# Kernel tuning notes

Hardware: AMD Instinct MI355X
Metric: run time of the kernel (lower is better)

## Reference

```python
import jax, jax.numpy as jnp
import numpy as np

NUM_LAYERS = 3


def setup_inputs() -> dict:
    key = jax.random.key(0)
    ks = jax.random.split(key, 12)
    N, E, D_IN, D, ED = 50000, 800000, 6, 64, 4
    return {
        "x": jax.random.normal(ks[0], (N, D_IN), dtype=jnp.float32),
        "edge_index": jax.random.randint(ks[1], (2, E), 0, N, dtype=jnp.int64),
        "edge_attr": jax.random.normal(ks[2], (E, ED), dtype=jnp.float32),
        "z_soft": jax.random.uniform(ks[3], (E, ED), dtype=jnp.float32),
        "W_nt": jax.random.normal(ks[4], (D, D_IN), dtype=jnp.float32) * 0.1,
        "b_nt": jax.random.normal(ks[5], (D,), dtype=jnp.float32) * 0.1,
        "weight": jax.random.normal(ks[6], (NUM_LAYERS, D, D), dtype=jnp.float32) * 0.1,
        "W_ih": jax.random.normal(ks[7], (3 * D, D), dtype=jnp.float32) * 0.1,
        "W_hh": jax.random.normal(ks[8], (3 * D, D), dtype=jnp.float32) * 0.1,
        "b_ih": jax.random.normal(ks[9], (3 * D,), dtype=jnp.float32) * 0.1,
        "b_hh": jax.random.normal(ks[10], (3 * D,), dtype=jnp.float32) * 0.1,
    }


def gru_cell(m, h, W_ih, W_hh, b_ih, b_hh):
    # PyTorch GRUCell: gates ordered (r, z, n)
    gi = m @ W_ih.T + b_ih
    gh = h @ W_hh.T + b_hh
    i_r, i_z, i_n = jnp.split(gi, 3, axis=-1)
    h_r, h_z, h_n = jnp.split(gh, 3, axis=-1)
    r = jax.nn.sigmoid(i_r + h_r)
    z = jax.nn.sigmoid(i_z + h_z)
    n = jnp.tanh(i_n + r * h_n)
    return (1.0 - z) * n + z * h


def reference(x, edge_index, edge_attr, z_soft, W_nt, b_nt, weight, W_ih, W_hh, b_ih, b_hh):
    # node_transform: Linear + ReLU
    h = jax.nn.relu(x @ W_nt.T + b_nt)  # [N, D]
    # edge_attr gating (faithful to source; unused since edge_weight=None)
    _ = z_soft * edge_attr
    src, dst = edge_index[0], edge_index[1]
    N = h.shape[0]
    for i in range(NUM_LAYERS):
        m = h @ weight[i]                                   # [N, D]
        agg = jax.ops.segment_sum(m[src], dst, num_segments=N)  # gather-scatter add
        h = gru_cell(agg, h, W_ih, W_hh, b_ih, b_hh)
    return h
```

## Files before the change

kernel.cpp:

```cpp
#include <hip/hip_runtime.h>
#include <hip/hip_bf16.h>
#include <stdint.h>

#define D 64
typedef __hip_bfloat16 bf16;
typedef unsigned short u16;
typedef __attribute__((ext_vector_type(8))) short bf16x8;
typedef __attribute__((ext_vector_type(4))) float f32x4;

__device__ __forceinline__ float bf2f(u16 u) { return __uint_as_float(((uint32_t)u) << 16); }
__device__ __forceinline__ u16 f2bf(float f) { return __bfloat16_as_ushort(__float2bfloat16(f)); }

template <bool F32>
__device__ __forceinline__ float ld(const void* p, int i) {
    if constexpr (F32) return ((const float*)p)[i];
    else return bf2f(((const u16*)p)[i]);
}

__global__ __launch_bounds__(256) void detect_kernel(const void* x, const int* ei, int* flags) {
    __shared__ float smax[256];
    __shared__ int sor[256];
    int t = threadIdx.x;
    const u16* xs = (const u16*)x;
    float mx = 0.f;
#pragma unroll
    for (int i = 0; i < 16; ++i) {
        float a = fabsf(bf2f(xs[t * 16 + i]));
        if (!(a == a)) a = 1e30f;
        mx = fmaxf(mx, a);
    }
    int any = 0;
#pragma unroll
    for (int i = 0; i < 8; ++i) any |= ei[2 * (t * 8 + i) + 1];
    smax[t] = mx; sor[t] = any;
    __syncthreads();
    for (int s = 128; s > 0; s >>= 1) {
        if (t < s) { smax[t] = fmaxf(smax[t], smax[t + s]); sor[t] |= sor[t + s]; }
        __syncthreads();
    }
    if (t == 0) { flags[0] = (smax[0] > 1000.f) ? 1 : 0; flags[1] = (sor[0] != 0) ? 1 : 0; }
}

__global__ __launch_bounds__(256) void convert_edges(const int* __restrict__ flags,
                                                     const int* __restrict__ ei,
                                                     uint32_t* __restrict__ pe, int E, int N) {
    int i0 = blockIdx.x * 1024 + threadIdx.x;
    bool i32 = flags[1] != 0;
#pragma unroll
    for (int u = 0; u < 4; ++u) {
        int i = i0 + u * 256;
        if (i < E) {
            int src, dst;
            if (i32) { src = ei[i];     dst = ei[E + i]; }
            else     { src = ei[2 * i]; dst = ei[2 * (E + i)]; }
            uint32_t v;
            if ((unsigned)src >= (unsigned)N || (unsigned)dst >= (unsigned)N) v = 0xFFFFFFFFu;
            else v = (uint32_t)(u16)src | ((uint32_t)dst << 16);
            pe[i] = v;
        }
    }
}

#define N_WCT 36864
#define N_WTH 12288
#define N_B   384
template <bool F32>
__device__ __forceinline__ void nt_body(const void* x, const void* Wnt, const void* bnt,
                                        u16* ht, int N, int blk) {
    int gid = blk * 256 + threadIdx.x;
    if (gid >= N * D) return;
    int n = gid >> 6, c = gid & 63;
    float acc = ld<F32>(bnt, c);
#pragma unroll
    for (int k = 0; k < 6; ++k)
        acc = fmaf(ld<F32>(x, n * 6 + k), ld<F32>(Wnt, c * 6 + k), acc);
    ht[gid] = f2bf(fmaxf(acc, 0.f));
}
template <bool F32>
__device__ __forceinline__ void wc_body(const void* W, const void* Wih, const void* Whh,
                                        const void* bih, const void* bhh,
                                        u16* WCh, u16* WCl, u16* WVh, u16* WVl,
                                        float* B, int blk) {
    int i = blk * 256 + threadIdx.x;
    if (i < N_WCT) {
        int l = i / 12288, rem = i % 12288, k = rem / 192, r = rem % 192;
        float acc = 0.f;
#pragma unroll 8
        for (int j = 0; j < 64; ++j)
            acc = fmaf(ld<F32>(W, l * 4096 + k * 64 + j), ld<F32>(Wih, r * 64 + j), acc);
        u16 hi = f2bf(acc);
        WCh[l * 12288 + r * 64 + k] = hi;
        WCl[l * 12288 + r * 64 + k] = f2bf(acc - bf2f(hi));
    } else if (i < N_WCT + N_WTH) {
        int rem = i - N_WCT;
        int k = rem / 192, r = rem % 192;
        float v = ld<F32>(Whh, r * 64 + k);
        u16 hi = f2bf(v);
        WVh[r * 64 + k] = hi;
        WVl[r * 64 + k] = f2bf(v - bf2f(hi));
    } else if (i < N_WCT + N_WTH + N_B) {
        int rem = i - N_WCT - N_WTH;
        B[rem] = (rem < 192) ? ld<F32>(bih, rem) : ld<F32>(bhh, rem - 192);
    }
}
__global__ __launch_bounds__(256) void prep_all(const int* __restrict__ flags,
                                                const void* x, const void* Wnt, const void* bnt,
                                                const void* W, const void* Wih, const void* Whh,
                                                const void* bih, const void* bhh,
                                                u16* ht, u16* WCh, u16* WCl, u16* WVh, u16* WVl,
                                                float* B,
                                                const uint32_t* __restrict__ pe,
                                                int* __restrict__ cnt,
                                                u16* __restrict__ ss16, int* __restrict__ novf,
                                                int* __restrict__ ovf,
                                                int E, int N, int NT_BLK, int WC_BLK, int EPS) {
    int b = blockIdx.x;
    if (b < NT_BLK) {
        if (flags[0]) nt_body<true>(x, Wnt, bnt, ht, N, b);
        else          nt_body<false>(x, Wnt, bnt, ht, N, b);
    } else if (b < NT_BLK + WC_BLK) {
        if (flags[0]) wc_body<true>(W, Wih, Whh, bih, bhh, WCh, WCl, WVh, WVl, B, b - NT_BLK);
        else          wc_body<false>(W, Wih, Whh, bih, bhh, WCh, WCl, WVh, WVl, B, b - NT_BLK);
    } else {
        int bf = b - NT_BLK - WC_BLK;
        unsigned shard = (unsigned)(b & 7);
        int beg = (bf >> 3) * EPS;
        int end = beg + EPS; if (end > E) end = E;
        for (int i = beg + (int)threadIdx.x; i < end; i += 256) {
            uint32_t e = pe[i];
            int dst = (int)(e >> 16);
            if ((((unsigned)dst >> 4) & 7u) != shard) continue;
            if (dst >= N) continue;
            int src = (int)(e & 0xffffu);
            int pos = atomicAdd(&cnt[dst], 1);
            if (pos < 64) ss16[(size_t)dst * 64 + pos] = (u16)src;
            else {
                int o = atomicAdd(novf, 1);
                if (o < E) { ovf[2 * o] = dst; ovf[2 * o + 1] = src; }
            }
        }
    }
}

#define NPB 16
#define LSTR 68

#define GPACK(P, JB, E0, E1) \
    _Pragma("unroll") for (int q_ = 0; q_ < 8; ++q_) { \
        int j_ = (JB) + 2 * q_ + half; \
        int ix_ = __shfl(iv[P], j_); \
        bool vq_ = j_ < dg[P]; \
        uint32_t d_ = htd[(uint32_t)(vq_ ? ix_ : 0) * 32u + (uint32_t)col]; \
        d_ = vq_ ? d_ : 0u; \
        E0 += __uint_as_float(d_ << 16); \
        E1 += __uint_as_float(d_ & 0xffff0000u); }

__global__ __launch_bounds__(256, 3) void layer_fused(const int* __restrict__ flags,
                                                   const u16* __restrict__ ht,
                                                   const int* __restrict__ cnt,
                                                   const u16* __restrict__ ss16,
                                                   const int* __restrict__ novf,
                                                   const int* __restrict__ ovf,
                                                   const u16* __restrict__ WCh,
                                                   const u16* __restrict__ WCl,
                                                   const u16* __restrict__ WVh,
                                                   const u16* __restrict__ WVl,
                                                   const float* __restrict__ B,
                                                   u16* __restrict__ houtb,
                                                   void* __restrict__ dout,
                                                   int N) {
    __shared__ alignas(16) float LA[NPB * LSTR];
    __shared__ alignas(16) float LH[NPB * LSTR];
    __shared__ alignas(16) u16 Ahi[NPB * 64];
    __shared__ alignas(16) u16 Alo[NPB * 64];
    __shared__ alignas(16) u16 Hb[NPB * 64];
    int t = threadIdx.x;
    int n0 = blockIdx.x * NPB;
    int lane = t & 63;
    int w = t >> 6;
    int w4 = w * 4;
    int half = lane >> 5;
    int col = lane & 31;
    const uint32_t* htd = (const uint32_t*)ht;

    {
        if (t < 128) {
            int row = t >> 3, c = (t & 7) * 8;
            bool v = (n0 + row) < N;
            uint4 vh = make_uint4(0u, 0u, 0u, 0u);
            if (v) vh = *(const uint4*)(ht + (size_t)(n0 + row) * D + c);
            float4 f0, f1;
            f0.x = bf2f((u16)(vh.x & 0xffff)); f0.y = bf2f((u16)(vh.x >> 16));
            f0.z = bf2f((u16)(vh.y & 0xffff)); f0.w = bf2f((u16)(vh.y >> 16));
            f1.x = bf2f((u16)(vh.z & 0xffff)); f1.y = bf2f((u16)(vh.z >> 16));
            f1.z = bf2f((u16)(vh.w & 0xffff)); f1.w = bf2f((u16)(vh.w >> 16));
            *(float4*)&LH[row * LSTR + c]     = f0;
            *(float4*)&LH[row * LSTR + c + 4] = f1;
            *(uint4*)((char*)Hb + row * 128 + ((c * 2) ^ ((row & 7) << 4))) = vh;
        }
    }

    int dg[4]; int iv[4];
#pragma unroll
    for (int p = 0; p < 4; ++p) {
        int n = n0 + w4 + p;
        dg[p] = 0; iv[p] = 0;
        if (n < N) {
            int c = cnt[n]; dg[p] = (c > 64) ? 64 : c;
            iv[p] = (int)ss16[(size_t)n * 64 + lane];
        }
    }
    float e00 = 0.f, e01 = 0.f, e10 = 0.f, e11 = 0.f;
    float e20 = 0.f, e21 = 0.f, e30 = 0.f, e31 = 0.f;
    GPACK(0, 0, e00, e01) GPACK(1, 0, e10, e11) GPACK(2, 0, e20, e21) GPACK(3, 0, e30, e31)
    if (dg[0] > 16) GPACK(0, 16, e00, e01)
    if (dg[1] > 16) GPACK(1, 16, e10, e11)
    if (dg[2] > 16) GPACK(2, 16, e20, e21)
    if (dg[3] > 16) GPACK(3, 16, e30, e31)
    e00 += __shfl_xor(e00, 32); e01 += __shfl_xor(e01, 32);
    e10 += __shfl_xor(e10, 32); e11 += __shfl_xor(e11, 32);
    e20 += __shfl_xor(e20, 32); e21 += __shfl_xor(e21, 32);
    e30 += __shfl_xor(e30, 32); e31 += __shfl_xor(e31, 32);
#define GTAIL(P, E0, E1) if (dg[P] > 32) { \
        for (int j = 32; j < dg[P]; ++j) { \
            uint32_t d_ = htd[(uint32_t)__shfl(iv[P], j) * 32u + (uint32_t)col]; \
            E0 += __uint_as_float(d_ << 16); \
            E1 += __uint_as_float(d_ & 0xffff0000u); } }
    GTAIL(0, e00, e01) GTAIL(1, e10, e11) GTAIL(2, e20, e21) GTAIL(3, e30, e31)
    if (half == 0) {
        float2 v0 = {e00, e01}, v1 = {e10, e11}, v2 = {e20, e21}, v3 = {e30, e31};
        *(float2*)&LA[(w4 + 0) * LSTR + 2 * col] = v0;
        *(float2*)&LA[(w4 + 1) * LSTR + 2 * col] = v1;
        *(float2*)&LA[(w4 + 2) * LSTR + 2 * col] = v2;
        *(float2*)&LA[(w4 + 3) * LSTR + 2 * col] = v3;
    }
    __syncthreads();
    {
        int nv = novf[0];
        if (nv > 0) {
            if (nv > (1 << 20)) nv = (1 << 20);
            for (int o = w; o < nv; o += 4) {
                int dst = ovf[2 * o];
                if (dst >= n0 && dst < n0 + NPB) {
                    int src = ovf[2 * o + 1];
                    atomicAdd(&LA[(dst - n0) * LSTR + lane], bf2f(ht[(size_t)src * D + lane]));
                }
            }
        }
    }
    __syncthreads();
    {
        int row = t >> 4, c = (t & 15) * 4;
        float4 v = *(const float4*)&LA[row * LSTR + c];
        u16 h0 = f2bf(v.x), h1 = f2bf(v.y), h2 = f2bf(v.z), h3 = f2bf(v.w);
        uint2 hh, llv;
        hh.x = (uint32_t)h0 | ((uint32_t)h1 << 16);
        hh.y = (uint32_t)h2 | ((uint32_t)h3 << 16);
        llv.x = (uint32_t)f2bf(v.x - bf2f(h0)) | ((uint32_t)f2bf(v.y - bf2f(h1)) << 16);
        llv.y = (uint32_t)f2bf(v.z - bf2f(h2)) | ((uint32_t)f2bf(v.w - bf2f(h3)) << 16);
        int off = row * 128 + ((c * 2) ^ ((row & 7) << 4));
        *(uint2*)((char*)Ahi + off) = hh;
        *(uint2*)((char*)Alo + off) = llv;
    }
    __syncthreads();

    int r = lane & 15, g = lane >> 4;
    int aoff0 = r * 128 + (((g * 16) + 0) ^ ((r & 7) << 4));
    int aoff1 = r * 128 + (((g * 16) + 64) ^ ((r & 7) << 4));
    bf16x8 aH0 = *(const bf16x8*)((const char*)Ahi + aoff0);
    bf16x8 aH1 = *(const bf16x8*)((const char*)Ahi + aoff1);
    bf16x8 aL0 = *(const bf16x8*)((const char*)Alo + aoff0);
    bf16x8 aL1 = *(const bf16x8*)((const char*)Alo + aoff1);
    bf16x8 hB0 = *(const bf16x8*)((const char*)Hb + aoff0);
    bf16x8 hB1 = *(const bf16x8*)((const char*)Hb + aoff1);

#define WFRAG(P, nt, ks) (*(const bf16x8*)((const char*)(P) + ((nt) * 16 + r) * 128 + (ks) * 64 + g * 16))
#define DO_TILE(nt, ai, ah) { \
    bf16x8 wch0 = WFRAG(WCh, nt, 0), wch1 = WFRAG(WCh, nt, 1); \
    bf16x8 wcl0 = WFRAG(WCl, nt, 0), wcl1 = WFRAG(WCl, nt, 1); \
    bf16x8 wvh0 = WFRAG(WVh, nt, 0), wvh1 = WFRAG(WVh, nt, 1); \
    bf16x8 wvl0 = WFRAG(WVl, nt, 0), wvl1 = WFRAG(WVl, nt, 1); \
    ai = __builtin_amdgcn_mfma_f32_16x16x32_bf16(aH0, wch0, ai, 0, 0, 0); \
    ai = __builtin_amdgcn_mfma_f32_16x16x32_bf16(aH1, wch1, ai, 0, 0, 0); \
    ai = __builtin_amdgcn_mfma_f32_16x16x32_bf16(aL0, wch0, ai, 0, 0, 0); \
    ai = __builtin_amdgcn_mfma_f32_16x16x32_bf16(aL1, wch1, ai, 0, 0, 0); \
    ai = __builtin_amdgcn_mfma_f32_16x16x32_bf16(aH0, wcl0, ai, 0, 0, 0); \
    ai = __builtin_amdgcn_mfma_f32_16x16x32_bf16(aH1, wcl1, ai, 0, 0, 0); \
    ah = __builtin_amdgcn_mfma_f32_16x16x32_bf16(hB0, wvh0, ah, 0, 0, 0); \
    ah = __builtin_amdgcn_mfma_f32_16x16x32_bf16(hB1, wvh1, ah, 0, 0, 0); \
    ah = __builtin_amdgcn_mfma_f32_16x16x32_bf16(hB0, wvl0, ah, 0, 0, 0); \
    ah = __builtin_amdgcn_mfma_f32_16x16x32_bf16(hB1, wvl1, ah, 0, 0, 0); }

    f32x4 air = {0.f, 0.f, 0.f, 0.f}, aiz = air, ain = air;
    f32x4 ahr = air, ahz = air, ahn = air;
    DO_TILE(w, air, ahr);
    DO_TILE(w + 4, aiz, ahz);
    DO_TILE(w + 8, ain, ahn);

    {
        int ch = w * 16 + r;
        float br = B[ch] + B[192 + ch];
        float bz = B[64 + ch] + B[256 + ch];
        float bi = B[128 + ch];
        float bh = B[320 + ch];
        int nb = g * 4;
#pragma unroll
        for (int j = 0; j < 4; ++j) {
            float gr = air[j] + ahr[j] + br;
            float gz = aiz[j] + ahz[j] + bz;
            float rr = 1.f / (1.f + __expf(-gr));
            float zz = 1.f / (1.f + __expf(-gz));
            float nx = ain[j] + bi + rr * (ahn[j] + bh);
            float th = 1.f - 2.f / (1.f + __expf(2.f * nx));
            float hold = LH[(nb + j) * LSTR + ch];
            LA[(nb + j) * LSTR + ch] = (1.f - zz) * th + zz * hold;
        }
    }
    __syncthreads();
    if (t < 128) {
        int row = t >> 3, c = (t & 7) * 8;
        int n = n0 + row;
        if (n < N) {
            float4 v0 = *(const float4*)&LA[row * LSTR + c];
            float4 v1 = *(const float4*)&LA[row * LSTR + c + 4];
            size_t idx = (size_t)n * D + c;
            if (houtb || !flags[0]) {
                uint4 o;
                o.x = (uint32_t)f2bf(v0.x) | ((uint32_t)f2bf(v0.y) << 16);
                o.y = (uint32_t)f2bf(v0.z) | ((uint32_t)f2bf(v0.w) << 16);
                o.z = (uint32_t)f2bf(v1.x) | ((uint32_t)f2bf(v1.y) << 16);
                o.w = (uint32_t)f2bf(v1.z) | ((uint32_t)f2bf(v1.w) << 16);
                if (houtb) *(uint4*)(houtb + idx) = o;
                else       *(uint4*)((u16*)dout + idx) = o;
            } else {
                *(float4*)((float*)dout + idx)     = v0;
                *(float4*)((float*)dout + idx + 4) = v1;
            }
        }
    }
}

extern "C" void kernel_launch(void* const* d_in, const int* in_sizes, int n_in,
                              void* d_out, int out_size, void* d_ws, size_t ws_size,
                              hipStream_t stream) {
    const void* x   = d_in[0];
    const int*  ei  = (const int*)d_in[1];
    const void* Wnt = d_in[4];
    const void* bnt = d_in[5];
    const void* Wt  = d_in[6];
    const void* Wih = d_in[7];
    const void* Whh = d_in[8];
    const void* bih = d_in[9];
    const void* bhh = d_in[10];

    int N = in_sizes[0] / 6;
    int E = in_sizes[1] / 2;
    int ND = N * D;

    int* flags = (int*)d_ws;
    float* B   = (float*)((char*)d_ws + 256);
    u16* WCh = (u16*)(B + N_B);
    u16* WCl = WCh + N_WCT;
    u16* WVh = WCl + N_WCT;
    u16* WVl = WVh + N_WTH;
    u16* htA = WVl + N_WTH;
    u16* htB = htA + ND;
    int* cnt  = (int*)(htB + ND);
    int* novf = cnt + N;
    u16* ss16 = (u16*)(novf + 1);
    int* ovf  = (int*)(ss16 + (size_t)N * 64);
    uint32_t* pe = (uint32_t*)(ovf + 2 * (size_t)E);

    int NT_BLK = (ND + 255) / 256;
    int WC_BLK = (N_WCT + N_WTH + N_B + 255) / 256;
    int FS = (E + 1023) / 1024;
    int EPS = (E + FS - 1) / FS;
    int FI_BLK = 8 * FS;
    int CV_BLK = (E + 1023) / 1024;

    hipMemsetAsync(cnt, 0, (size_t)(N + 1) * sizeof(int), stream);
    detect_kernel<<<1, 256, 0, stream>>>(x, ei, flags);
    convert_edges<<<CV_BLK, 256, 0, stream>>>(flags, ei, pe, E, N);
    prep_all<<<NT_BLK + WC_BLK + FI_BLK, 256, 0, stream>>>(flags, x, Wnt, bnt, Wt, Wih, Whh,
                                                           bih, bhh, htA, WCh, WCl, WVh, WVl, B,
                                                           pe, cnt, ss16, novf, ovf,
                                                           E, N, NT_BLK, WC_BLK, EPS);

    u16* hcur = htA;
    u16* hnxt = htB;
    for (int layer = 0; layer < 3; ++layer) {
        bool last = (layer == 2);
        layer_fused<<<(N + NPB - 1) / NPB, 256, 0, stream>>>(flags, hcur, cnt, ss16, novf, ovf,
                                                             WCh + layer * 12288, WCl + layer * 12288,
                                                             WVh, WVl, B,
                                                             last ? nullptr : hnxt,
                                                             last ? d_out : nullptr, N);
        u16* t = hcur; hcur = hnxt; hnxt = t;
    }
}
```

Baseline: 299.1 us.

## Use scalar neighbor-index loads with zero sentinel row instead of shuffles

The gather in the layer kernel now reads packed neighbor indices directly as wave-uniform scalar loads instead of loading them per lane and broadcasting with shuffles. Empty adjacency slots are pre-filled with 0xFFFF and clamped to N, which points at an extra all-zero row appended to each hidden-state buffer, so the per-edge validity select goes away. The overflow buffer is capped at a fixed size, the wave index is made uniform with readfirstlane, and the launch-bounds occupancy hint is dropped. The cost is an extra memset of the whole slot table per call and a hard cap on overflow edges.

```diff
diff --git a/kernel.cpp b/kernel.cpp
--- a/kernel.cpp
+++ b/kernel.cpp
@@ -7,6 +7,8 @@
 typedef unsigned short u16;
 typedef __attribute__((ext_vector_type(8))) short bf16x8;
 typedef __attribute__((ext_vector_type(4))) float f32x4;
+
+#define OVF_CAP 65536
 
 __device__ __forceinline__ float bf2f(u16 u) { return __uint_as_float(((uint32_t)u) << 16); }
 __device__ __forceinline__ u16 f2bf(float f) { return __bfloat16_as_ushort(__float2bfloat16(f)); }
@@ -136,7 +138,7 @@
             if (pos < 64) ss16[(size_t)dst * 64 + pos] = (u16)src;
             else {
                 int o = atomicAdd(novf, 1);
-                if (o < E) { ovf[2 * o] = dst; ovf[2 * o + 1] = src; }
+                if (o < OVF_CAP) { ovf[2 * o] = dst; ovf[2 * o + 1] = src; }
             }
         }
     }
@@ -145,17 +147,43 @@
 #define NPB 16
 #define LSTR 68
 
-#define GPACK(P, JB, E0, E1) \
-    _Pragma("unroll") for (int q_ = 0; q_ < 8; ++q_) { \
-        int j_ = (JB) + 2 * q_ + half; \
-        int ix_ = __shfl(iv[P], j_); \
-        bool vq_ = j_ < dg[P]; \
-        uint32_t d_ = htd[(uint32_t)(vq_ ? ix_ : 0) * 32u + (uint32_t)col]; \
-        d_ = vq_ ? d_ : 0u; \
+#define SGATH(P, E0, E1) { \
+    int nu_ = n0 + w4 + P; \
+    int dgp_ = 0; \
+    if (nu_ < N) { \
+        dgp_ = cnt[nu_]; if (dgp_ > 64) dgp_ = 64; \
+        const uint32_t* bpd_ = (const uint32_t*)(ss16 + (size_t)nu_ * 64); \
+        _Pragma("unroll") for (int q_ = 0; q_ < 8; ++q_) { \
+            uint32_t wq_ = bpd_[q_]; \
+            int ixE_ = (int)(wq_ & 0xffffu); if (ixE_ > N) ixE_ = N; \
+            int ixO_ = (int)(wq_ >> 16);     if (ixO_ > N) ixO_ = N; \
+            int ix_ = half ? ixO_ : ixE_; \
+            uint32_t d_ = htd[(uint32_t)ix_ * 32u + (uint32_t)col]; \
+            E0 += __uint_as_float(d_ << 16); \
+            E1 += __uint_as_float(d_ & 0xffff0000u); } \
+        if (dgp_ > 16) { \
+            _Pragma("unroll") for (int q_ = 8; q_ < 16; ++q_) { \
+                uint32_t wq_ = bpd_[q_]; \
+                int ixE_ = (int)(wq_ & 0xffffu); if (ixE_ > N) ixE_ = N; \
+                int ixO_ = (int)(wq_ >> 16);     if (ixO_ > N) ixO_ = N; \
+                int ix_ = half ? ixO_ : ixE_; \
+                uint32_t d_ = htd[(uint32_t)ix_ * 32u + (uint32_t)col]; \
+                E0 += __uint_as_float(d_ << 16); \
+                E1 += __uint_as_float(d_ & 0xffff0000u); } } \
+    } \
+    dgs[P] = dgp_; }
+
+#define GTAIL(P, E0, E1) if (dgs[P] > 32) { \
+    const uint32_t* bpd_ = (const uint32_t*)(ss16 + (size_t)(n0 + w4 + P) * 64); \
+    for (int j = 32; j < dgs[P]; ++j) { \
+        uint32_t wq_ = bpd_[j >> 1]; \
+        int ix_ = (j & 1) ? (int)(wq_ >> 16) : (int)(wq_ & 0xffffu); \
+        if (ix_ > N) ix_ = N; \
+        uint32_t d_ = htd[(uint32_t)ix_ * 32u + (uint32_t)col]; \
         E0 += __uint_as_float(d_ << 16); \
-        E1 += __uint_as_float(d_ & 0xffff0000u); }
-
-__global__ __launch_bounds__(256, 3) void layer_fused(const int* __restrict__ flags,
+        E1 += __uint_as_float(d_ & 0xffff0000u); } }
+
+__global__ __launch_bounds__(256) void layer_fused(const int* __restrict__ flags,
                                                    const u16* __restrict__ ht,
                                                    const int* __restrict__ cnt,
                                                    const u16* __restrict__ ss16,
@@ -177,8 +205,8 @@
     int t = threadIdx.x;
     int n0 = blockIdx.x * NPB;
     int lane = t & 63;
-    int w = t >> 6;
-    int w4 = w * 4;
+    int w4 = __builtin_amdgcn_readfirstlane(t >> 6) * 4;
+    int wv = w4 >> 2;
     int half = lane >> 5;
     int col = lane & 31;
     const uint32_t* htd = (const uint32_t*)ht;
@@ -200,32 +228,14 @@
         }
     }
 
-    int dg[4]; int iv[4];
-#pragma unroll
-    for (int p = 0; p < 4; ++p) {
-        int n = n0 + w4 + p;
-        dg[p] = 0; iv[p] = 0;
-        if (n < N) {
-            int c = cnt[n]; dg[p] = (c > 64) ? 64 : c;
-            iv[p] = (int)ss16[(size_t)n * 64 + lane];
-        }
-    }
+    int dgs[4];
     float e00 = 0.f, e01 = 0.f, e10 = 0.f, e11 = 0.f;
     float e20 = 0.f, e21 = 0.f, e30 = 0.f, e31 = 0.f;
-    GPACK(0, 0, e00, e01) GPACK(1, 0, e10, e11) GPACK(2, 0, e20, e21) GPACK(3, 0, e30, e31)
-    if (dg[0] > 16) GPACK(0, 16, e00, e01)
-    if (dg[1] > 16) GPACK(1, 16, e10, e11)
-    if (dg[2] > 16) GPACK(2, 16, e20, e21)
-    if (dg[3] > 16) GPACK(3, 16, e30, e31)
+    SGATH(0, e00, e01) SGATH(1, e10, e11) SGATH(2, e20, e21) SGATH(3, e30, e31)
     e00 += __shfl_xor(e00, 32); e01 += __shfl_xor(e01, 32);
     e10 += __shfl_xor(e10, 32); e11 += __shfl_xor(e11, 32);
     e20 += __shfl_xor(e20, 32); e21 += __shfl_xor(e21, 32);
     e30 += __shfl_xor(e30, 32); e31 += __shfl_xor(e31, 32);
-#define GTAIL(P, E0, E1) if (dg[P] > 32) { \
-        for (int j = 32; j < dg[P]; ++j) { \
-            uint32_t d_ = htd[(uint32_t)__shfl(iv[P], j) * 32u + (uint32_t)col]; \
-            E0 += __uint_as_float(d_ << 16); \
-            E1 += __uint_as_float(d_ & 0xffff0000u); } }
     GTAIL(0, e00, e01) GTAIL(1, e10, e11) GTAIL(2, e20, e21) GTAIL(3, e30, e31)
     if (half == 0) {
         float2 v0 = {e00, e01}, v1 = {e10, e11}, v2 = {e20, e21}, v3 = {e30, e31};
@@ -238,8 +248,8 @@
     {
         int nv = novf[0];
         if (nv > 0) {
-            if (nv > (1 << 20)) nv = (1 << 20);
-            for (int o = w; o < nv; o += 4) {
+            if (nv > OVF_CAP) nv = OVF_CAP;
+            for (int o = wv; o < nv; o += 4) {
                 int dst = ovf[2 * o];
                 if (dst >= n0 && dst < n0 + NPB) {
                     int src = ovf[2 * o + 1];
@@ -293,12 +303,12 @@
 
     f32x4 air = {0.f, 0.f, 0.f, 0.f}, aiz = air, ain = air;
     f32x4 ahr = air, ahz = air, ahn = air;
-    DO_TILE(w, air, ahr);
-    DO_TILE(w + 4, aiz, ahz);
-    DO_TILE(w + 8, ain, ahn);
+    DO_TILE(wv, air, ahr);
+    DO_TILE(wv + 4, aiz, ahz);
+    DO_TILE(wv + 8, ain, ahn);
 
     {
-        int ch = w * 16 + r;
+        int ch = wv * 16 + r;
         float br = B[ch] + B[192 + ch];
         float bz = B[64 + ch] + B[256 + ch];
         float bi = B[128 + ch];
@@ -364,12 +374,12 @@
     u16* WVh = WCl + N_WCT;
     u16* WVl = WVh + N_WTH;
     u16* htA = WVl + N_WTH;
-    u16* htB = htA + ND;
-    int* cnt  = (int*)(htB + ND);
+    u16* htB = htA + ND + D;
+    int* cnt  = (int*)(htB + ND + D);
     int* novf = cnt + N;
     u16* ss16 = (u16*)(novf + 1);
     int* ovf  = (int*)(ss16 + (size_t)N * 64);
-    uint32_t* pe = (uint32_t*)(ovf + 2 * (size_t)E);
+    uint32_t* pe = (uint32_t*)(ovf + 2 * (size_t)OVF_CAP);
 
     int NT_BLK = (ND + 255) / 256;
     int WC_BLK = (N_WCT + N_WTH + N_B + 255) / 256;
@@ -379,6 +389,9 @@
     int CV_BLK = (E + 1023) / 1024;
 
     hipMemsetAsync(cnt, 0, (size_t)(N + 1) * sizeof(int), stream);
+    hipMemsetAsync(ss16, 0xFF, (size_t)N * 128, stream);
+    hipMemsetAsync(htA + (size_t)ND, 0, D * sizeof(u16), stream);
+    hipMemsetAsync(htB + (size_t)ND, 0, D * sizeof(u16), stream);
     detect_kernel<<<1, 256, 0, stream>>>(x, ei, flags);
     convert_edges<<<CV_BLK, 256, 0, stream>>>(flags, ei, pe, E, N);
     prep_all<<<NT_BLK + WC_BLK + FI_BLK, 256, 0, stream>>>(flags, x, Wnt, bnt, Wt, Wih, Whh,
```

After: 313.8 us. 4.9% more time.
